# Kernel tuning notes

Hardware: AMD Instinct MI355X
Metric: run time of the kernel (lower is better)

Reference implementation:

```python
import jax, jax.numpy as jnp
import numpy as np

EPS = 0.1
MAX_ITER = 100
THRESH = 0.1


def setup_inputs() -> dict:
    key = jax.random.key(0)
    k1, k2 = jax.random.split(key)
    N = 4096
    x = jax.random.normal(k1, (N, N), dtype=jnp.float32)
    y = jax.random.normal(k2, (N, N), dtype=jnp.float32)
    return {"x": x, "y": y}


def _sinkhorn(x, y):
    # forward softmaxes inputs along last dim
    x = jax.nn.softmax(x, axis=-1)
    y = jax.nn.softmax(y, axis=-1)
    # squared-euclidean cost |x_i - y_j|^2, expanded to avoid an [N,N,D] broadcast
    x2 = jnp.sum(x * x, axis=-1)  # [n]
    y2 = jnp.sum(y * y, axis=-1)  # [m]
    C = x2[:, None] + y2[None, :] - 2.0 * (x @ y.T)  # [n, m]
    n = x.shape[-1]  # source sizes mu/nu by the FEATURE dim (requires n == m == d)
    log_mu = jnp.log(jnp.full((n,), 1.0 / n, dtype=C.dtype) + 1e-8)
    log_nu = log_mu

    def M(u, v):
        # faithful to source: both u and v broadcast over the COLUMN axis
        return (-C + u[None, :] + v[None, :]) / EPS

    def step(carry, _):
        u, v, done = carry
        u1 = u
        u_new = EPS * (log_mu - jax.nn.logsumexp(M(u, v), axis=-1)) + u
        v_new = EPS * (log_nu - jax.nn.logsumexp(M(u_new, v).T, axis=-1)) + v
        # torch: (u-u1).abs().sum(-1).mean() with implicit batch of 1 == plain sum
        err = jnp.sum(jnp.abs(u_new - u1))
        u = jnp.where(done, u, u_new)
        v = jnp.where(done, v, v_new)
        return (u, v, done | (err < THRESH)), None

    init = (jnp.zeros((n,), C.dtype), jnp.zeros((n,), C.dtype), jnp.array(False))
    (u, v, _), _ = jax.lax.scan(step, init, None, length=MAX_ITER)
    pi = jnp.exp(M(u, v))  # [n, m] (torch returns [1, n, m]; batch dim squeezed)
    cost = jnp.sum(pi * C)  # cost.mean() over the singleton batch == scalar sum
    return cost, pi, C


def reference(x, y):
    return _sinkhorn(x, y)
```

## Files before the change

kernel.cpp:

```cpp
#include <hip/hip_runtime.h>
#include <math.h>

#define NN 4096

typedef __bf16 bf16;
typedef __attribute__((ext_vector_type(8))) __bf16 bf16x8;
typedef __attribute__((ext_vector_type(4))) float f32x4;

__device__ __forceinline__ void gld16(const void* g, void* l) {
  __builtin_amdgcn_global_load_lds((const __attribute__((address_space(1))) void*)g,
                                   (__attribute__((address_space(3))) void*)l, 16, 0, 0);
}


__device__ __forceinline__ double blockSumD(double v) {
  __shared__ double w[4];
  #pragma unroll
  for (int o = 32; o > 0; o >>= 1) v += __shfl_down(v, o, 64);
  __syncthreads();
  if ((threadIdx.x & 63) == 0) w[threadIdx.x >> 6] = v;
  __syncthreads();
  return w[0] + w[1] + w[2] + w[3];
}

__device__ __forceinline__ float blockMaxF(float v) {
  __shared__ float w[4];
  #pragma unroll
  for (int o = 32; o > 0; o >>= 1) v = fmaxf(v, __shfl_down(v, o, 64));
  __syncthreads();
  if ((threadIdx.x & 63) == 0) w[threadIdx.x >> 6] = v;
  __syncthreads();
  return fmaxf(fmaxf(w[0], w[1]), fmaxf(w[2], w[3]));
}


__global__ void softmax_rows(const float* __restrict__ x, const float* __restrict__ y,
                             bf16* __restrict__ xh, bf16* __restrict__ yh,
                             float* __restrict__ rowsq) {
  int row = blockIdx.x;
  int r = (row < NN) ? row : row - NN;
  const float* __restrict__ src = (row < NN) ? x : y;
  bf16* __restrict__ dst = (row < NN) ? xh : yh;
  size_t base = (size_t)r * NN;
  int t = threadIdx.x;

  float v[16];
  float m = -3.402823466e38f;
  #pragma unroll
  for (int j = 0; j < 16; ++j) {
    v[j] = src[base + t + 256 * j];
    m = fmaxf(m, v[j]);
  }
  float M = blockMaxF(m);

  double s = 0.0;
  #pragma unroll
  for (int j = 0; j < 16; ++j) {
    v[j] = expf(v[j] - M);
    s += (double)v[j];
  }
  double S = blockSumD(s);
  double inv = 1.0 / S;

  double q = 0.0;
  #pragma unroll
  for (int j = 0; j < 16; ++j) {
    float p = (float)((double)v[j] * inv);
    dst[base + t + 256 * j] = (bf16)p;
    q += (double)p * (double)p;
  }
  double Q = blockSumD(q);
  if (t == 0) rowsq[row] = (float)Q;
}


__global__ __launch_bounds__(256) void gemm_bt(const bf16* __restrict__ A,
                                               const bf16* __restrict__ B,
                                               const float* __restrict__ rowsq,
                                               float* __restrict__ C) {
  __shared__ __align__(16) bf16 As[128 * 64];
  __shared__ __align__(16) bf16 Bs[128 * 64];
  int t = threadIdx.x;
  int i0 = blockIdx.y * 128;
  int j0 = blockIdx.x * 128;
  int w = t >> 6, l = t & 63;
  int mrow = (w >> 1) * 64, ncol = (w & 1) * 64;
  int lr = l & 15, lq = l >> 4;

  f32x4 acc[4][4] = {};

  for (int kc = 0; kc < NN; kc += 64) {
    __syncthreads();
    #pragma unroll
    for (int q = 0; q < 4; ++q) {
      int c = t + 256 * q;
      int row = c >> 3;
      int jg = (c & 7) ^ (row & 7);
      gld16(A + (size_t)(i0 + row) * NN + kc + jg * 8, (char*)As + c * 16);
    }
    #pragma unroll
    for (int q = 0; q < 4; ++q) {
      int c = t + 256 * q;
      int row = c >> 3;
      int jg = (c & 7) ^ (row & 7);
      gld16(B + (size_t)(j0 + row) * NN + kc + jg * 8, (char*)Bs + c * 16);
    }
    __syncthreads();

    #pragma unroll
    for (int s = 0; s < 2; ++s) {
      bf16x8 af[4], bg[4];
      #pragma unroll
      for (int i = 0; i < 4; ++i) {
        int ra = mrow + 16 * i + lr;
        int ja = (s * 4 + lq) ^ (ra & 7);
        af[i] = *(const bf16x8*)((const char*)As + (ra * 8 + ja) * 16);
        int rb = ncol + 16 * i + lr;
        int jb = (s * 4 + lq) ^ (rb & 7);
        bg[i] = *(const bf16x8*)((const char*)Bs + (rb * 8 + jb) * 16);
      }
      #pragma unroll
      for (int i = 0; i < 4; ++i)
        #pragma unroll
        for (int jj = 0; jj < 4; ++jj)
          acc[i][jj] = __builtin_amdgcn_mfma_f32_16x16x32_bf16(af[i], bg[jj], acc[i][jj], 0, 0, 0);
    }
  }

  float y2v[4];
  #pragma unroll
  for (int jj = 0; jj < 4; ++jj) y2v[jj] = rowsq[NN + j0 + ncol + 16 * jj + lr];
  #pragma unroll
  for (int i = 0; i < 4; ++i) {
    #pragma unroll
    for (int r = 0; r < 4; ++r) {
      int grow = i0 + mrow + 16 * i + lq * 4 + r;
      float x2 = rowsq[grow];
      size_t rowoff = (size_t)grow * NN + j0 + ncol;
      #pragma unroll
      for (int jj = 0; jj < 4; ++jj)
        C[rowoff + 16 * jj + lr] = x2 + y2v[jj] - 2.0f * acc[i][jj][r];
    }
  }
}


__global__ void col_lse_partial(const float* __restrict__ C, double* __restrict__ part) {
  int col = blockIdx.x * 256 + threadIdx.x;
  int r0 = blockIdx.y * 128;
  double s = 0.0;
  for (int r = 0; r < 128; ++r) {
    float c = C[(size_t)(r0 + r) * NN + col];
    s += exp(((double)(-c)) / 0.1);
  }
  part[(size_t)blockIdx.y * NN + col] = s;
}


__global__ void col_lse_final(const double* __restrict__ part, double* __restrict__ sd) {
  int col = blockIdx.x * 256 + threadIdx.x;
  double s = 0.0;
  #pragma unroll
  for (int ch = 0; ch < 32; ++ch) s += part[(size_t)ch * NN + col];
  double log_nu = log(1.0 / (double)NN + 1e-8);
  sd[col] = log_nu - log(s);
}


__global__ void pi_cost(const float* __restrict__ Cm, const double* __restrict__ sd,
                        float* __restrict__ pi, double* __restrict__ costpart) {
  size_t idx0 = (size_t)blockIdx.x * 2048 + threadIdx.x;
  double acc = 0.0;
  #pragma unroll
  for (int j = 0; j < 8; ++j) {
    size_t idx = idx0 + 256 * j;
    float c = Cm[idx];
    int col = (int)(idx & (NN - 1));
    double m = ((double)(-c)) / 0.1 + sd[col];
    double p = exp(m);
    pi[idx] = (float)p;
    acc += p * (double)c;
  }
  double total = blockSumD(acc);
  if (threadIdx.x == 0) costpart[blockIdx.x] = total;
}


__global__ void cost_final(const double* __restrict__ costpart, float* __restrict__ out) {
  double s = 0.0;
  #pragma unroll
  for (int j = 0; j < 32; ++j) s += costpart[threadIdx.x + 256 * j];
  double total = blockSumD(s);
  if (threadIdx.x == 0) out[0] = (float)total;
}


extern "C" void kernel_launch(void* const* d_in, const int* in_sizes, int n_in,
                              void* d_out, int out_size, void* d_ws, size_t ws_size,
                              hipStream_t stream) {
  const float* x = (const float*)d_in[0];
  const float* y = (const float*)d_in[1];
  float* out = (float*)d_out;
  float* pi = out + 1;
  float* Cm = out + 1 + (size_t)NN * NN;

  char* ws = (char*)d_ws;
  bf16* xh = (bf16*)ws;
  bf16* yh = xh + (size_t)NN * NN;
  size_t off = (size_t)NN * NN * 2 * 2;
  float* rowsq = (float*)(ws + off);       off += 2 * NN * 4;
  double* sd = (double*)(ws + off);        off += NN * 8;
  double* costpart = (double*)(ws + off);  off += 8192 * 8;

  double* colpart = (double*)((char*)d_out + 66060288);

  hipLaunchKernelGGL(softmax_rows, dim3(2 * NN), dim3(256), 0, stream, x, y, xh, yh, rowsq);
  hipLaunchKernelGGL(gemm_bt, dim3(32, 32), dim3(256), 0, stream, xh, yh, rowsq, Cm);
  hipLaunchKernelGGL(col_lse_partial, dim3(16, 32), dim3(256), 0, stream, Cm, colpart);
  hipLaunchKernelGGL(col_lse_final, dim3(16), dim3(256), 0, stream, colpart, sd);
  hipLaunchKernelGGL(pi_cost, dim3(8192), dim3(256), 0, stream, Cm, sd, pi, costpart);
  hipLaunchKernelGGL(cost_final, dim3(1), dim3(256), 0, stream, costpart, out);
}
```

Measured before the change: 449.3 us.

## Fuse column exp-sum into GEMM epilogue and drop double precision in elementwise passes

```diff
diff --git a/kernel.cpp b/kernel.cpp
--- a/kernel.cpp
+++ b/kernel.cpp
@@ -4,6 +4,7 @@
 #define NN 4096
 
 typedef __bf16 bf16;
+typedef __attribute__((ext_vector_type(4))) __bf16 bf16x4;
 typedef __attribute__((ext_vector_type(8))) __bf16 bf16x8;
 typedef __attribute__((ext_vector_type(4))) float f32x4;
 
@@ -39,37 +40,39 @@
                              float* __restrict__ rowsq) {
   int row = blockIdx.x;
   int r = (row < NN) ? row : row - NN;
-  const float* __restrict__ src = (row < NN) ? x : y;
-  bf16* __restrict__ dst = (row < NN) ? xh : yh;
-  size_t base = (size_t)r * NN;
+  const f32x4* __restrict__ src = (const f32x4*)(((row < NN) ? x : y) + (size_t)r * NN);
+  bf16x4* __restrict__ dst = (bf16x4*)(((row < NN) ? xh : yh) + (size_t)r * NN);
   int t = threadIdx.x;
 
-  float v[16];
+  f32x4 v[4];
   float m = -3.402823466e38f;
   #pragma unroll
-  for (int j = 0; j < 16; ++j) {
-    v[j] = src[base + t + 256 * j];
-    m = fmaxf(m, v[j]);
+  for (int j = 0; j < 4; ++j) {
+    v[j] = src[t + 256 * j];
+    m = fmaxf(fmaxf(fmaxf(m, v[j].x), fmaxf(v[j].y, v[j].z)), v[j].w);
   }
   float M = blockMaxF(m);
 
-  double s = 0.0;
-  #pragma unroll
-  for (int j = 0; j < 16; ++j) {
-    v[j] = expf(v[j] - M);
-    s += (double)v[j];
-  }
-  double S = blockSumD(s);
-  double inv = 1.0 / S;
-
-  double q = 0.0;
-  #pragma unroll
-  for (int j = 0; j < 16; ++j) {
-    float p = (float)((double)v[j] * inv);
-    dst[base + t + 256 * j] = (bf16)p;
-    q += (double)p * (double)p;
-  }
-  double Q = blockSumD(q);
+  float s = 0.0f;
+  #pragma unroll
+  for (int j = 0; j < 4; ++j) {
+    v[j].x = expf(v[j].x - M); v[j].y = expf(v[j].y - M);
+    v[j].z = expf(v[j].z - M); v[j].w = expf(v[j].w - M);
+    s += (v[j].x + v[j].y) + (v[j].z + v[j].w);
+  }
+  double S = blockSumD((double)s);
+  float inv = (float)(1.0 / S);
+
+  float q = 0.0f;
+  #pragma unroll
+  for (int j = 0; j < 4; ++j) {
+    f32x4 p = v[j] * inv;
+    bf16x4 h;
+    h.x = (bf16)p.x; h.y = (bf16)p.y; h.z = (bf16)p.z; h.w = (bf16)p.w;
+    dst[t + 256 * j] = h;
+    q += (p.x * p.x + p.y * p.y) + (p.z * p.z + p.w * p.w);
+  }
+  double Q = blockSumD((double)q);
   if (t == 0) rowsq[row] = (float)Q;
 }
 
@@ -77,9 +80,11 @@
 __global__ __launch_bounds__(256) void gemm_bt(const bf16* __restrict__ A,
                                                const bf16* __restrict__ B,
                                                const float* __restrict__ rowsq,
-                                               float* __restrict__ C) {
+                                               float* __restrict__ C,
+                                               float* __restrict__ colpart) {
   __shared__ __align__(16) bf16 As[128 * 64];
   __shared__ __align__(16) bf16 Bs[128 * 64];
+  __shared__ float lsc[2][128];
   int t = threadIdx.x;
   int i0 = blockIdx.y * 128;
   int j0 = blockIdx.x * 128;
@@ -127,7 +132,7 @@
     }
   }
 
-  float y2v[4];
+  float y2v[4], ec[4] = {0.f, 0.f, 0.f, 0.f};
   #pragma unroll
   for (int jj = 0; jj < 4; ++jj) y2v[jj] = rowsq[NN + j0 + ncol + 16 * jj + lr];
   #pragma unroll
@@ -138,50 +143,51 @@
       float x2 = rowsq[grow];
       size_t rowoff = (size_t)grow * NN + j0 + ncol;
       #pragma unroll
-      for (int jj = 0; jj < 4; ++jj)
-        C[rowoff + 16 * jj + lr] = x2 + y2v[jj] - 2.0f * acc[i][jj][r];
-    }
-  }
-}
-
-
-__global__ void col_lse_partial(const float* __restrict__ C, double* __restrict__ part) {
-  int col = blockIdx.x * 256 + threadIdx.x;
-  int r0 = blockIdx.y * 128;
-  double s = 0.0;
-  for (int r = 0; r < 128; ++r) {
-    float c = C[(size_t)(r0 + r) * NN + col];
-    s += exp(((double)(-c)) / 0.1);
-  }
-  part[(size_t)blockIdx.y * NN + col] = s;
-}
-
-
-__global__ void col_lse_final(const double* __restrict__ part, double* __restrict__ sd) {
+      for (int jj = 0; jj < 4; ++jj) {
+        float cv = x2 + y2v[jj] - 2.0f * acc[i][jj][r];
+        C[rowoff + 16 * jj + lr] = cv;
+        ec[jj] += expf(-10.0f * cv);
+      }
+    }
+  }
+  #pragma unroll
+  for (int jj = 0; jj < 4; ++jj) {
+    ec[jj] += __shfl_xor(ec[jj], 16, 64);
+    ec[jj] += __shfl_xor(ec[jj], 32, 64);
+  }
+  if (lq == 0) {
+    #pragma unroll
+    for (int jj = 0; jj < 4; ++jj) lsc[w >> 1][ncol + 16 * jj + lr] = ec[jj];
+  }
+  __syncthreads();
+  if (t < 128) colpart[(size_t)blockIdx.y * NN + j0 + t] = lsc[0][t] + lsc[1][t];
+}
+
+
+__global__ void col_lse_final(const float* __restrict__ colpart, float* __restrict__ sdf) {
   int col = blockIdx.x * 256 + threadIdx.x;
   double s = 0.0;
   #pragma unroll
-  for (int ch = 0; ch < 32; ++ch) s += part[(size_t)ch * NN + col];
+  for (int ch = 0; ch < 32; ++ch) s += (double)colpart[(size_t)ch * NN + col];
   double log_nu = log(1.0 / (double)NN + 1e-8);
-  sd[col] = log_nu - log(s);
-}
-
-
-__global__ void pi_cost(const float* __restrict__ Cm, const double* __restrict__ sd,
+  sdf[col] = (float)(log_nu - log(s));
+}
+
+
+__global__ void pi_cost(const float* __restrict__ Cm, const float* __restrict__ sdf,
                         float* __restrict__ pi, double* __restrict__ costpart) {
   size_t idx0 = (size_t)blockIdx.x * 2048 + threadIdx.x;
-  double acc = 0.0;
+  float facc = 0.0f;
   #pragma unroll
   for (int j = 0; j < 8; ++j) {
     size_t idx = idx0 + 256 * j;
     float c = Cm[idx];
     int col = (int)(idx & (NN - 1));
-    double m = ((double)(-c)) / 0.1 + sd[col];
-    double p = exp(m);
-    pi[idx] = (float)p;
-    acc += p * (double)c;
-  }
-  double total = blockSumD(acc);
+    float p = expf(fmaf(-10.0f, c, sdf[col]));
+    pi[idx] = p;
+    facc = fmaf(p, c, facc);
+  }
+  double total = blockSumD((double)facc);
   if (threadIdx.x == 0) costpart[blockIdx.x] = total;
 }
 
@@ -209,15 +215,13 @@
   bf16* yh = xh + (size_t)NN * NN;
   size_t off = (size_t)NN * NN * 2 * 2;
   float* rowsq = (float*)(ws + off);       off += 2 * NN * 4;
-  double* sd = (double*)(ws + off);        off += NN * 8;
+  float* sdf = (float*)(ws + off);         off += NN * 4;
+  float* colpart = (float*)(ws + off);     off += 32 * NN * 4;
   double* costpart = (double*)(ws + off);  off += 8192 * 8;
 
-  double* colpart = (double*)((char*)d_out + 66060288);
-
   hipLaunchKernelGGL(softmax_rows, dim3(2 * NN), dim3(256), 0, stream, x, y, xh, yh, rowsq);
-  hipLaunchKernelGGL(gemm_bt, dim3(32, 32), dim3(256), 0, stream, xh, yh, rowsq, Cm);
-  hipLaunchKernelGGL(col_lse_partial, dim3(16, 32), dim3(256), 0, stream, Cm, colpart);
-  hipLaunchKernelGGL(col_lse_final, dim3(16), dim3(256), 0, stream, colpart, sd);
-  hipLaunchKernelGGL(pi_cost, dim3(8192), dim3(256), 0, stream, Cm, sd, pi, costpart);
+  hipLaunchKernelGGL(gemm_bt, dim3(32, 32), dim3(256), 0, stream, xh, yh, rowsq, Cm, colpart);
+  hipLaunchKernelGGL(col_lse_final, dim3(16), dim3(256), 0, stream, colpart, sdf);
+  hipLaunchKernelGGL(pi_cost, dim3(8192), dim3(256), 0, stream, Cm, sdf, pi, costpart);
   hipLaunchKernelGGL(cost_final, dim3(1), dim3(256), 0, stream, costpart, out);
 }
```

Result: faster. 398.7 us (-11.3%).
